# Performance work log

Measured on AMD Instinct MI355X. Metric: run time of the kernel, lower is better.

Reference implementation:

```python
import jax, jax.numpy as jnp
import numpy as np

EPS = 1e-12

def _l2norm(v):
    return v / (jnp.linalg.norm(v) + EPS)

def _spectral_norm_weight(W, u):
    # torch spectral_norm with n_power_iterations=1: v = norm(W^T u); u' = norm(W v);
    # sigma = u'^T W v with u', v detached; returns W / sigma.
    v = jax.lax.stop_gradient(_l2norm(W.T @ u))
    u2 = jax.lax.stop_gradient(_l2norm(W @ v))
    sigma = u2 @ (W @ v)
    return W / sigma

def setup_inputs() -> dict:
    key = jax.random.key(0)
    ks = jax.random.split(key, 8)
    C, H, W = 64, 96, 96
    Cfg = C // 8
    g = 1e-2  # small weight scale (module uses orthogonal init with tiny gain)
    return {
        "x":  jax.random.normal(ks[0], (1, C, H, W), jnp.float32),
        "Wf": jax.random.normal(ks[1], (Cfg, C), jnp.float32) * g,
        "bf": jnp.zeros((Cfg,), jnp.float32),
        "Wg": jax.random.normal(ks[2], (Cfg, C), jnp.float32) * g,
        "bg": jnp.zeros((Cfg,), jnp.float32),
        "Wh": jax.random.normal(ks[3], (C, C), jnp.float32) * g,
        "bh": jnp.zeros((C,), jnp.float32),
        "gamma": jax.random.normal(ks[4], (1,), jnp.float32),
        "uf": jax.random.normal(ks[5], (Cfg,), jnp.float32),
        "ug": jax.random.normal(ks[6], (Cfg,), jnp.float32),
        "uh": jax.random.normal(ks[7], (C,), jnp.float32),
    }

def reference(x, Wf, bf, Wg, bg, Wh, bh, gamma, uf, ug, uh):
    B, C, H, Wd = x.shape
    N = H * Wd
    xf = x.reshape(B, C, N)  # 1x1 convs act per-pixel -> matmul over channel dim
    Wf_sn = _spectral_norm_weight(Wf, uf)
    Wg_sn = _spectral_norm_weight(Wg, ug)
    Wh_sn = _spectral_norm_weight(Wh, uh)
    f_flat = jnp.einsum('oc,bcn->bon', Wf_sn, xf) + bf[:, None]  # [B,Cfg,N]
    g_flat = jnp.einsum('oc,bcn->bon', Wg_sn, xf) + bg[:, None]  # [B,Cfg,N]
    h_flat = jnp.einsum('oc,bcn->bon', Wh_sn, xf) + bh[:, None]  # [B,C,N]
    # s[b,n,m] = sum_k g[b,k,n] * f[b,k,m]  (g^T f)
    s = jnp.einsum('bkn,bkm->bnm', g_flat, f_flat)  # [B,N,N]
    beta = jax.nn.softmax(s, axis=1)                # softmax over dim=1 (g axis)
    o = jnp.einsum('bcn,bnm->bcm', h_flat, beta)    # [B,C,N]
    o = o.reshape(B, C, H, Wd)
    return gamma * o + x
```

## Files before the change

### kernel.cpp

```cpp
#include <hip/hip_runtime.h>
#include <hip/hip_bf16.h>

#define NPIX 9216
#define MTILES (NPIX / 16)

typedef __attribute__((ext_vector_type(4))) float f32x4;
typedef __attribute__((ext_vector_type(8))) short bf16x8;
typedef __attribute__((ext_vector_type(2))) unsigned int u32x2;

__device__ __forceinline__ void gload_lds16(const void* g, void* l) {
  __builtin_amdgcn_global_load_lds(
      (const __attribute__((address_space(1))) unsigned int*)g,
      (__attribute__((address_space(3))) unsigned int*)l, 16, 0, 0);
}
__device__ __forceinline__ void gload_lds4(const void* g, void* l) {
  __builtin_amdgcn_global_load_lds(
      (const __attribute__((address_space(1))) unsigned int*)g,
      (__attribute__((address_space(3))) unsigned int*)l, 4, 0, 0);
}
#define LDS_OFF(p) ((unsigned)(unsigned long long)(const __attribute__((address_space(3))) char*)(const char*)(p))

__global__ __launch_bounds__(256) void spectral_kernel(
    const float* __restrict__ Wf, const float* __restrict__ bfv,
    const float* __restrict__ Wg, const float* __restrict__ bgv,
    const float* __restrict__ Wh, const float* __restrict__ bhv,
    const float* __restrict__ uf, const float* __restrict__ ug,
    const float* __restrict__ uh,
    float* __restrict__ Wsc, float* __restrict__ bsc) {
  __shared__ float vsh3[3][64];
  __shared__ float is_s[3];
  const int tid = threadIdx.x;
  const int wv = tid >> 6, t = tid & 63;
  if (wv < 3) {
    const float* W = (wv == 0) ? Wf : (wv == 1) ? Wg : Wh;
    const float* u = (wv == 0) ? uf : (wv == 1) ? ug : uh;
    const int O = (wv == 2) ? 64 : 8;
    float v = 0.f;
    for (int o = 0; o < O; ++o) v += W[o * 64 + t] * u[o];
    float s = v * v;
    for (int off = 32; off; off >>= 1) s += __shfl_xor(s, off);
    vsh3[wv][t] = v / (sqrtf(s) + 1e-12f);
    float wvv = 0.f;
    if (t < O) { for (int c = 0; c < 64; ++c) wvv += W[t * 64 + c] * vsh3[wv][c]; }
    float s2 = (t < O) ? wvv * wvv : 0.f;
    for (int off = 32; off; off >>= 1) s2 += __shfl_xor(s2, off);
    const float nw = sqrtf(s2);
    if (t == 0) is_s[wv] = (nw + 1e-12f) / s2;
  }
  __syncthreads();
  const float sf = is_s[0] * 0.25f, sg = is_s[1], sh = is_s[2];
  for (int e = tid; e < 5120; e += 256) {
    const int r = e >> 6, c = e & 63;
    float val;
    if (r < 8)       val = Wf[r * 64 + c] * sf;
    else if (r < 16) val = Wg[(r - 8) * 64 + c] * sg;
    else             val = Wh[(r - 16) * 64 + c] * sh;
    Wsc[e] = val;
  }
  if (tid < 80) {
    bsc[tid] = (tid < 8) ? bfv[tid] * 0.25f
             : (tid < 16) ? bgv[tid - 8] : bhv[tid - 16];
  }
}

__global__ __launch_bounds__(256) void fgh_kernel(
    const float* __restrict__ x,
    const float* __restrict__ Wsc, const float* __restrict__ bsc,
    ushort* __restrict__ Qp, ushort* __restrict__ Kp, ushort* __restrict__ Vt2) {
  const int tid = threadIdx.x;
  const int px = tid & 63;
  const int rw = __builtin_amdgcn_readfirstlane(tid >> 6);
  const int r0 = blockIdx.y * 16 + rw * 4;
  const int p  = blockIdx.x * 64 + px;

  float xv[64];
  #pragma unroll
  for (int c = 0; c < 64; ++c) xv[c] = x[c * NPIX + p];

  float acc0 = 0.f, acc1 = 0.f, acc2 = 0.f, acc3 = 0.f;
  const float* w0 = Wsc + (r0 + 0) * 64;
  const float* w1 = Wsc + (r0 + 1) * 64;
  const float* w2 = Wsc + (r0 + 2) * 64;
  const float* w3 = Wsc + (r0 + 3) * 64;
  #pragma unroll
  for (int c = 0; c < 64; ++c) {
    const float xc = xv[c];
    acc0 += w0[c] * xc; acc1 += w1[c] * xc;
    acc2 += w2[c] * xc; acc3 += w3[c] * xc;
  }

  const int tile = p >> 5, nt = p & 31;
  const int tt = nt >> 4, gg = (nt >> 2) & 3, ii = nt & 3;
  const int kbase = tile * 512 + nt * 8;
  float accs[4] = {acc0, acc1, acc2, acc3};
  #pragma unroll
  for (int j = 0; j < 4; ++j) {
    const int r = r0 + j;
    const float val = accs[j] + bsc[r];
    if (r < 8) {
      const __hip_bfloat16 h = __float2bfloat16(val);
      const float hf = __bfloat162float(h);
      const __hip_bfloat16 lo = __float2bfloat16(val - hf);
      Qp[p * 16 + r]     = *(const ushort*)&h;
      Qp[p * 16 + 8 + r] = *(const ushort*)&lo;
    } else if (r < 16) {
      const int rk = r - 8;
      const __hip_bfloat16 h = __float2bfloat16(val);
      const float hf = __bfloat162float(h);
      const __hip_bfloat16 lo = __float2bfloat16(val - hf);
      Kp[kbase + rk]       = *(const ushort*)&h;
      Kp[kbase + 256 + rk] = *(const ushort*)&lo;
    } else {
      const int rv = r - 16;
      const __hip_bfloat16 hv = __float2bfloat16(val);
      const int idx = tile * 2048 +
          ((rv * 32 + gg * 8 + tt * 4 + ii) ^ (((rv >> 1) & 7) << 3));
      Vt2[idx] = *(const ushort*)&hv;
    }
  }
}

template <int S>
__global__ __launch_bounds__(256) void attn_kernel(
    const ushort* __restrict__ Qp, const ushort* __restrict__ Kp,
    const ushort* __restrict__ Vt2,
    ushort* __restrict__ Om,
    float* __restrict__ Sm) {
  constexpr int NSEG = NPIX / S;
  constexpr int NT = NSEG / 32;
  __shared__ ushort Vs[4][2048];
  __shared__ ushort Ks[4][512];
  const int tid  = threadIdx.x;
  const int w    = tid >> 6;
  const int l    = tid & 63;
  const int mloc = l & 15;
  const int g    = l >> 4;
  const int spl  = blockIdx.y;
  const int mrow = blockIdx.x * 64 + w * 16 + mloc;

  bf16x8 qh = *(const bf16x8*)(Qp + mrow * 16);
  bf16x8 ql = *(const bf16x8*)(Qp + mrow * 16 + 8);
  asm volatile("" : "+v"(qh), "+v"(ql));

  const int n0 = spl * NSEG;
  const char* vsrc = (const char*)Vt2 + ((size_t)(n0 >> 5)) * 4096 + w * 1024 + l * 16;
  const char* ksrc = (const char*)Kp + ((size_t)(n0 >> 5)) * 1024 + w * 256 + l * 4;

  #define STAGE(t_) do {                                                  \
    const int b_ = (t_) & 3;                                              \
    gload_lds16(vsrc + (size_t)(t_) * 4096, (char*)&Vs[b_][0] + w * 1024);\
    gload_lds4 (ksrc + (size_t)(t_) * 1024, (char*)&Ks[b_][0] + w * 256); \
  } while (0)

  STAGE(0);
  STAGE(1);

  const unsigned ks_base = LDS_OFF(&Ks[0][0]);
  const unsigned vs_base = LDS_OFF(&Vs[0][0]);
  const unsigned vswz = (mloc * 64 + g * 16) ^ (((mloc >> 1) & 7) << 4);

  float mx = -INFINITY, ls = 0.f;
  const f32x4 zero = {0.f, 0.f, 0.f, 0.f};
  f32x4 acc0 = zero, acc1 = zero, acc2 = zero, acc3 = zero;

  for (int t = 0; t < NT; ++t) {
    const int b = t & 3;
    if (t + 2 < NT) {
      STAGE(t + 2);
      asm volatile("s_waitcnt vmcnt(4)" ::: "memory");
    } else if (t + 1 < NT) {
      asm volatile("s_waitcnt vmcnt(2)" ::: "memory");
    } else {
      asm volatile("s_waitcnt vmcnt(0)" ::: "memory");
    }
    __builtin_amdgcn_s_barrier();

    const unsigned kaddr = ks_base + b * 1024 + mloc * 16;
    const unsigned vaddr = vs_base + b * 4096 + vswz;
    bf16x8 kh0, kl0, kh1, kl1, v0, v1, v2, v3;
    asm volatile("ds_read_b128 %0, %1"            : "=v"(kh0) : "v"(kaddr));
    asm volatile("ds_read_b128 %0, %1 offset:256" : "=v"(kh1) : "v"(kaddr));
    asm volatile("ds_read_b128 %0, %1 offset:512" : "=v"(kl0) : "v"(kaddr));
    asm volatile("ds_read_b128 %0, %1 offset:768" : "=v"(kl1) : "v"(kaddr));
    asm volatile("ds_read_b128 %0, %1"            : "=v"(v0)  : "v"(vaddr));
    asm volatile("ds_read_b128 %0, %1 offset:1024": "=v"(v1)  : "v"(vaddr));
    asm volatile("ds_read_b128 %0, %1 offset:2048": "=v"(v2)  : "v"(vaddr));
    asm volatile("ds_read_b128 %0, %1 offset:3072": "=v"(v3)  : "v"(vaddr));
    asm volatile("s_waitcnt lgkmcnt(0)" ::: "memory");
    __builtin_amdgcn_sched_barrier(0);

    f32x4 s0 = zero, s1 = zero;
    s0 = __builtin_amdgcn_mfma_f32_16x16x32_bf16(kh0, qh, s0, 0, 0, 0);
    s1 = __builtin_amdgcn_mfma_f32_16x16x32_bf16(kh1, qh, s1, 0, 0, 0);
    s0 = __builtin_amdgcn_mfma_f32_16x16x32_bf16(kh0, ql, s0, 0, 0, 0);
    s1 = __builtin_amdgcn_mfma_f32_16x16x32_bf16(kh1, ql, s1, 0, 0, 0);
    s0 = __builtin_amdgcn_mfma_f32_16x16x32_bf16(kl0, qh, s0, 0, 0, 0);
    s1 = __builtin_amdgcn_mfma_f32_16x16x32_bf16(kl1, qh, s1, 0, 0, 0);

    const float tm = fmaxf(
        fmaxf(fmaxf(s0[0], s0[1]), fmaxf(s0[2], s0[3])),
        fmaxf(fmaxf(s1[0], s1[1]), fmaxf(s1[2], s1[3])));
    if (__any(tm > mx + 8.0f)) {
      float tr = fmaxf(tm, __shfl_xor(tm, 16));
      tr = fmaxf(tr, __shfl_xor(tr, 32));
      const float mxn = fmaxf(mx, tr);
      const float corr = __expf(mx - mxn);
      ls *= corr;
      const float c0 = __shfl(corr, (g << 2) + 0);
      const float c1 = __shfl(corr, (g << 2) + 1);
      const float c2 = __shfl(corr, (g << 2) + 2);
      const float c3 = __shfl(corr, (g << 2) + 3);
      acc0[0] *= c0; acc0[1] *= c1; acc0[2] *= c2; acc0[3] *= c3;
      acc1[0] *= c0; acc1[1] *= c1; acc1[2] *= c2; acc1[3] *= c3;
      acc2[0] *= c0; acc2[1] *= c1; acc2[2] *= c2; acc2[3] *= c3;
      acc3[0] *= c0; acc3[1] *= c1; acc3[2] *= c2; acc3[3] *= c3;
      mx = mxn;
    }
    float pj[8];
    pj[0] = __expf(s0[0] - mx); pj[1] = __expf(s0[1] - mx);
    pj[2] = __expf(s0[2] - mx); pj[3] = __expf(s0[3] - mx);
    pj[4] = __expf(s1[0] - mx); pj[5] = __expf(s1[1] - mx);
    pj[6] = __expf(s1[2] - mx); pj[7] = __expf(s1[3] - mx);
    ls += ((pj[0] + pj[1]) + (pj[2] + pj[3])) + ((pj[4] + pj[5]) + (pj[6] + pj[7]));

    union { unsigned int u[4]; bf16x8 v; } pu;
    #pragma unroll
    for (int jj = 0; jj < 4; ++jj) {
      unsigned int r;
      asm("v_cvt_pk_bf16_f32 %0, %1, %2" : "=v"(r) : "v"(pj[2 * jj]), "v"(pj[2 * jj + 1]));
      pu.u[jj] = r;
    }
    acc0 = __builtin_amdgcn_mfma_f32_16x16x32_bf16(pu.v, v0, acc0, 0, 0, 0);
    acc1 = __builtin_amdgcn_mfma_f32_16x16x32_bf16(pu.v, v1, acc1, 0, 0, 0);
    acc2 = __builtin_amdgcn_mfma_f32_16x16x32_bf16(pu.v, v2, acc2, 0, 0, 0);
    acc3 = __builtin_amdgcn_mfma_f32_16x16x32_bf16(pu.v, v3, acc3, 0, 0, 0);
  }
  #undef STAGE

  ls += __shfl_xor(ls, 16);
  ls += __shfl_xor(ls, 32);

  const size_t mt = (size_t)blockIdx.x * 4 + w;
  ushort* Ob = Om + (mt * S + spl) * 1024;
  float*  Sb = Sm + (mt * S + spl) * 32;
  #pragma unroll
  for (int ct = 0; ct < 4; ++ct) {
    const f32x4 a = (ct == 0) ? acc0 : (ct == 1) ? acc1 : (ct == 2) ? acc2 : acc3;
    unsigned int r0, r1;
    asm("v_cvt_pk_bf16_f32 %0, %1, %2" : "=v"(r0) : "v"(a[0]), "v"(a[1]));
    asm("v_cvt_pk_bf16_f32 %0, %1, %2" : "=v"(r1) : "v"(a[2]), "v"(a[3]));
    u32x2 pk; pk[0] = r0; pk[1] = r1;
    *(u32x2*)(Ob + (ct * 16 + mloc) * 16 + 4 * g) = pk;
  }
  if (l < 16) { Sb[l] = mx; Sb[16 + l] = ls; }
}

template <int S>
__global__ __launch_bounds__(256) void combine_kernel(
    const ushort* __restrict__ Om, const float* __restrict__ Sm,
    const float* __restrict__ x, const float* __restrict__ gammap,
    float* __restrict__ out) {
  const int mt = blockIdx.x;
  const int m0 = mt * 16;
  const float gamma = gammap[0];
  const float* Sb = Sm + (size_t)mt * S * 32;
  const ushort* Ob = Om + (size_t)mt * S * 1024;
  for (int e = threadIdx.x; e < 1024; e += 256) {
    const int m = e & 15, c = e >> 4;
    float M = -INFINITY;
    #pragma unroll
    for (int s = 0; s < S; ++s) M = fmaxf(M, Sb[s * 32 + m]);
    float L = 0.f, val = 0.f;
    #pragma unroll
    for (int s = 0; s < S; ++s) {
      const float wgt = __expf(Sb[s * 32 + m] - M);
      L += Sb[s * 32 + 16 + m] * wgt;
      union { unsigned int i; float f; } cv;
      cv.i = ((unsigned int)Ob[s * 1024 + e]) << 16;
      val += cv.f * wgt;
    }
    const int idx = c * NPIX + m0 + m;
    out[idx] = gamma * (val / L) + x[idx];
  }
}

extern "C" void kernel_launch(void* const* d_in, const int* in_sizes, int n_in,
                              void* d_out, int out_size, void* d_ws, size_t ws_size,
                              hipStream_t stream) {
  const float* x     = (const float*)d_in[0];
  const float* Wf    = (const float*)d_in[1];
  const float* bf    = (const float*)d_in[2];
  const float* Wg    = (const float*)d_in[3];
  const float* bg    = (const float*)d_in[4];
  const float* Wh    = (const float*)d_in[5];
  const float* bh    = (const float*)d_in[6];
  const float* gamma = (const float*)d_in[7];
  const float* uf    = (const float*)d_in[8];
  const float* ug    = (const float*)d_in[9];
  const float* uh    = (const float*)d_in[10];
  float* out = (float*)d_out;

  char* ws = (char*)d_ws;
  float*  Wsc = (float*)(ws);
  float*  bsc = (float*)(ws + 20480);
  ushort* Qp  = (ushort*)(ws + 21504);
  ushort* Kp  = (ushort*)(ws + 21504 + NPIX * 16 * 2);
  ushort* Vt2 = (ushort*)(ws + 21504 + 2 * NPIX * 16 * 2);
  const size_t off = 21504 + (size_t)2 * NPIX * 16 * 2 + (size_t)NPIX * 64 * 2;
  ushort* Om = (ushort*)(ws + off);
  const size_t need16 = off + (size_t)MTILES * 16 * 1024 * 2 + (size_t)MTILES * 16 * 32 * 4;

  spectral_kernel<<<1, 256, 0, stream>>>(Wf, bf, Wg, bg, Wh, bh, uf, ug, uh, Wsc, bsc);
  fgh_kernel<<<dim3(NPIX / 64, 5), 256, 0, stream>>>(x, Wsc, bsc, Qp, Kp, Vt2);
  if (ws_size >= need16) {
    float* Sm = (float*)(ws + off + (size_t)MTILES * 16 * 1024 * 2);
    attn_kernel<16><<<dim3(NPIX / 64, 16), 256, 0, stream>>>(Qp, Kp, Vt2, Om, Sm);
    combine_kernel<16><<<MTILES, 256, 0, stream>>>(Om, Sm, x, gamma, out);
  } else {
    float* Sm = (float*)(ws + off + (size_t)MTILES * 8 * 1024 * 2);
    attn_kernel<8><<<dim3(NPIX / 64, 8), 256, 0, stream>>>(Qp, Kp, Vt2, Om, Sm);
    combine_kernel<8><<<MTILES, 256, 0, stream>>>(Om, Sm, x, gamma, out);
  }
}
```

Before: 77.60 us.

## Fuse spectral norm into projection, use exp2 softmax, split LDS wait, widen combine grid

Every projection block now recomputes the spectral-norm power iteration itself, which removes the separate single-block launch and the scaled-weight workspace round trip. Q is prescaled by log2(e) so the softmax and the combine step use exp2f, and the rescale threshold is adjusted to match. The attention loop now waits only for the K reads before the score MFMAs and waits for the V reads after the softmax, so LDS latency can overlap with the exp work. The combine kernel launches four times as many blocks, one element per thread. The cost is redundant spectral-norm work in every projection block.

```diff
diff --git a/kernel.cpp b/kernel.cpp
--- a/kernel.cpp
+++ b/kernel.cpp
@@ -20,13 +20,14 @@
 }
 #define LDS_OFF(p) ((unsigned)(unsigned long long)(const __attribute__((address_space(3))) char*)(const char*)(p))
 
-__global__ __launch_bounds__(256) void spectral_kernel(
+__global__ __launch_bounds__(256) void fgh_kernel(
+    const float* __restrict__ x,
     const float* __restrict__ Wf, const float* __restrict__ bfv,
     const float* __restrict__ Wg, const float* __restrict__ bgv,
     const float* __restrict__ Wh, const float* __restrict__ bhv,
     const float* __restrict__ uf, const float* __restrict__ ug,
     const float* __restrict__ uh,
-    float* __restrict__ Wsc, float* __restrict__ bsc) {
+    ushort* __restrict__ Qp, ushort* __restrict__ Kp, ushort* __restrict__ Vt2) {
   __shared__ float vsh3[3][64];
   __shared__ float is_s[3];
   const int tid = threadIdx.x;
@@ -48,26 +49,8 @@
     if (t == 0) is_s[wv] = (nw + 1e-12f) / s2;
   }
   __syncthreads();
-  const float sf = is_s[0] * 0.25f, sg = is_s[1], sh = is_s[2];
-  for (int e = tid; e < 5120; e += 256) {
-    const int r = e >> 6, c = e & 63;
-    float val;
-    if (r < 8)       val = Wf[r * 64 + c] * sf;
-    else if (r < 16) val = Wg[(r - 8) * 64 + c] * sg;
-    else             val = Wh[(r - 16) * 64 + c] * sh;
-    Wsc[e] = val;
-  }
-  if (tid < 80) {
-    bsc[tid] = (tid < 8) ? bfv[tid] * 0.25f
-             : (tid < 16) ? bgv[tid - 8] : bhv[tid - 16];
-  }
-}
-
-__global__ __launch_bounds__(256) void fgh_kernel(
-    const float* __restrict__ x,
-    const float* __restrict__ Wsc, const float* __restrict__ bsc,
-    ushort* __restrict__ Qp, ushort* __restrict__ Kp, ushort* __restrict__ Vt2) {
-  const int tid = threadIdx.x;
+
+  const float LOG2E = 1.44269504f;
   const int px = tid & 63;
   const int rw = __builtin_amdgcn_readfirstlane(tid >> 6);
   const int r0 = blockIdx.y * 16 + rw * 4;
@@ -77,27 +60,30 @@
   #pragma unroll
   for (int c = 0; c < 64; ++c) xv[c] = x[c * NPIX + p];
 
-  float acc0 = 0.f, acc1 = 0.f, acc2 = 0.f, acc3 = 0.f;
-  const float* w0 = Wsc + (r0 + 0) * 64;
-  const float* w1 = Wsc + (r0 + 1) * 64;
-  const float* w2 = Wsc + (r0 + 2) * 64;
-  const float* w3 = Wsc + (r0 + 3) * 64;
+  const float* W0;
+  float scl;
+  if (r0 < 8)       { W0 = Wf + r0 * 64;        scl = is_s[0]; }
+  else if (r0 < 16) { W0 = Wg + (r0 - 8) * 64;  scl = is_s[1]; }
+  else              { W0 = Wh + (r0 - 16) * 64; scl = is_s[2]; }
+
+  float acc[4] = {0.f, 0.f, 0.f, 0.f};
   #pragma unroll
   for (int c = 0; c < 64; ++c) {
     const float xc = xv[c];
-    acc0 += w0[c] * xc; acc1 += w1[c] * xc;
-    acc2 += w2[c] * xc; acc3 += w3[c] * xc;
+    acc[0] += W0[c]       * xc;
+    acc[1] += W0[64 + c]  * xc;
+    acc[2] += W0[128 + c] * xc;
+    acc[3] += W0[192 + c] * xc;
   }
 
   const int tile = p >> 5, nt = p & 31;
   const int tt = nt >> 4, gg = (nt >> 2) & 3, ii = nt & 3;
   const int kbase = tile * 512 + nt * 8;
-  float accs[4] = {acc0, acc1, acc2, acc3};
   #pragma unroll
   for (int j = 0; j < 4; ++j) {
     const int r = r0 + j;
-    const float val = accs[j] + bsc[r];
     if (r < 8) {
+      const float val = (acc[j] * scl + bfv[r]) * 0.25f * LOG2E;
       const __hip_bfloat16 h = __float2bfloat16(val);
       const float hf = __bfloat162float(h);
       const __hip_bfloat16 lo = __float2bfloat16(val - hf);
@@ -105,6 +91,7 @@
       Qp[p * 16 + 8 + r] = *(const ushort*)&lo;
     } else if (r < 16) {
       const int rk = r - 8;
+      const float val = acc[j] * scl + bgv[rk];
       const __hip_bfloat16 h = __float2bfloat16(val);
       const float hf = __bfloat162float(h);
       const __hip_bfloat16 lo = __float2bfloat16(val - hf);
@@ -112,12 +99,52 @@
       Kp[kbase + 256 + rk] = *(const ushort*)&lo;
     } else {
       const int rv = r - 16;
+      const float val = acc[j] * scl + bhv[rv];
       const __hip_bfloat16 hv = __float2bfloat16(val);
       const int idx = tile * 2048 +
           ((rv * 32 + gg * 8 + tt * 4 + ii) ^ (((rv >> 1) & 7) << 3));
       Vt2[idx] = *(const ushort*)&hv;
     }
   }
+}
+
+__device__ __forceinline__ void softmax_step(
+    const f32x4 s0, const f32x4 s1, int g, float& mx, float& ls,
+    f32x4& a0, f32x4& a1, f32x4& a2, f32x4& a3, bf16x8& pv) {
+  const float m1 = fmaxf(fmaxf(s0[0], s0[1]), s0[2]);
+  const float m2 = fmaxf(fmaxf(s0[3], s1[0]), s1[1]);
+  const float m3 = fmaxf(fmaxf(s1[2], s1[3]), m1);
+  const float tm = fmaxf(m2, m3);
+  if (__any(tm > mx + 11.5416f)) {
+    float tr = fmaxf(tm, __shfl_xor(tm, 16));
+    tr = fmaxf(tr, __shfl_xor(tr, 32));
+    const float mxn = fmaxf(mx, tr);
+    const float corr = exp2f(mx - mxn);
+    ls *= corr;
+    const float c0 = __shfl(corr, (g << 2) + 0);
+    const float c1 = __shfl(corr, (g << 2) + 1);
+    const float c2 = __shfl(corr, (g << 2) + 2);
+    const float c3 = __shfl(corr, (g << 2) + 3);
+    a0[0] *= c0; a0[1] *= c1; a0[2] *= c2; a0[3] *= c3;
+    a1[0] *= c0; a1[1] *= c1; a1[2] *= c2; a1[3] *= c3;
+    a2[0] *= c0; a2[1] *= c1; a2[2] *= c2; a2[3] *= c3;
+    a3[0] *= c0; a3[1] *= c1; a3[2] *= c2; a3[3] *= c3;
+    mx = mxn;
+  }
+  float pj[8];
+  pj[0] = exp2f(s0[0] - mx); pj[1] = exp2f(s0[1] - mx);
+  pj[2] = exp2f(s0[2] - mx); pj[3] = exp2f(s0[3] - mx);
+  pj[4] = exp2f(s1[0] - mx); pj[5] = exp2f(s1[1] - mx);
+  pj[6] = exp2f(s1[2] - mx); pj[7] = exp2f(s1[3] - mx);
+  ls += ((pj[0] + pj[1]) + (pj[2] + pj[3])) + ((pj[4] + pj[5]) + (pj[6] + pj[7]));
+  union { unsigned int u[4]; bf16x8 v; } pu;
+  #pragma unroll
+  for (int jj = 0; jj < 4; ++jj) {
+    unsigned int r;
+    asm("v_cvt_pk_bf16_f32 %0, %1, %2" : "=v"(r) : "v"(pj[2 * jj]), "v"(pj[2 * jj + 1]));
+    pu.u[jj] = r;
+  }
+  pv = pu.v;
 }
 
 template <int S>
@@ -186,7 +213,7 @@
     asm volatile("ds_read_b128 %0, %1 offset:1024": "=v"(v1)  : "v"(vaddr));
     asm volatile("ds_read_b128 %0, %1 offset:2048": "=v"(v2)  : "v"(vaddr));
     asm volatile("ds_read_b128 %0, %1 offset:3072": "=v"(v3)  : "v"(vaddr));
-    asm volatile("s_waitcnt lgkmcnt(0)" ::: "memory");
+    asm volatile("s_waitcnt lgkmcnt(4)" ::: "memory");
     __builtin_amdgcn_sched_barrier(0);
 
     f32x4 s0 = zero, s1 = zero;
@@ -197,43 +224,15 @@
     s0 = __builtin_amdgcn_mfma_f32_16x16x32_bf16(kl0, qh, s0, 0, 0, 0);
     s1 = __builtin_amdgcn_mfma_f32_16x16x32_bf16(kl1, qh, s1, 0, 0, 0);
 
-    const float tm = fmaxf(
-        fmaxf(fmaxf(s0[0], s0[1]), fmaxf(s0[2], s0[3])),
-        fmaxf(fmaxf(s1[0], s1[1]), fmaxf(s1[2], s1[3])));
-    if (__any(tm > mx + 8.0f)) {
-      float tr = fmaxf(tm, __shfl_xor(tm, 16));
-      tr = fmaxf(tr, __shfl_xor(tr, 32));
-      const float mxn = fmaxf(mx, tr);
-      const float corr = __expf(mx - mxn);
-      ls *= corr;
-      const float c0 = __shfl(corr, (g << 2) + 0);
-      const float c1 = __shfl(corr, (g << 2) + 1);
-      const float c2 = __shfl(corr, (g << 2) + 2);
-      const float c3 = __shfl(corr, (g << 2) + 3);
-      acc0[0] *= c0; acc0[1] *= c1; acc0[2] *= c2; acc0[3] *= c3;
-      acc1[0] *= c0; acc1[1] *= c1; acc1[2] *= c2; acc1[3] *= c3;
-      acc2[0] *= c0; acc2[1] *= c1; acc2[2] *= c2; acc2[3] *= c3;
-      acc3[0] *= c0; acc3[1] *= c1; acc3[2] *= c2; acc3[3] *= c3;
-      mx = mxn;
-    }
-    float pj[8];
-    pj[0] = __expf(s0[0] - mx); pj[1] = __expf(s0[1] - mx);
-    pj[2] = __expf(s0[2] - mx); pj[3] = __expf(s0[3] - mx);
-    pj[4] = __expf(s1[0] - mx); pj[5] = __expf(s1[1] - mx);
-    pj[6] = __expf(s1[2] - mx); pj[7] = __expf(s1[3] - mx);
-    ls += ((pj[0] + pj[1]) + (pj[2] + pj[3])) + ((pj[4] + pj[5]) + (pj[6] + pj[7]));
-
-    union { unsigned int u[4]; bf16x8 v; } pu;
-    #pragma unroll
-    for (int jj = 0; jj < 4; ++jj) {
-      unsigned int r;
-      asm("v_cvt_pk_bf16_f32 %0, %1, %2" : "=v"(r) : "v"(pj[2 * jj]), "v"(pj[2 * jj + 1]));
-      pu.u[jj] = r;
-    }
-    acc0 = __builtin_amdgcn_mfma_f32_16x16x32_bf16(pu.v, v0, acc0, 0, 0, 0);
-    acc1 = __builtin_amdgcn_mfma_f32_16x16x32_bf16(pu.v, v1, acc1, 0, 0, 0);
-    acc2 = __builtin_amdgcn_mfma_f32_16x16x32_bf16(pu.v, v2, acc2, 0, 0, 0);
-    acc3 = __builtin_amdgcn_mfma_f32_16x16x32_bf16(pu.v, v3, acc3, 0, 0, 0);
+    bf16x8 pv;
+    softmax_step(s0, s1, g, mx, ls, acc0, acc1, acc2, acc3, pv);
+
+    asm volatile("s_waitcnt lgkmcnt(0)" ::: "memory");
+    __builtin_amdgcn_sched_barrier(0);
+    acc0 = __builtin_amdgcn_mfma_f32_16x16x32_bf16(pv, v0, acc0, 0, 0, 0);
+    acc1 = __builtin_amdgcn_mfma_f32_16x16x32_bf16(pv, v1, acc1, 0, 0, 0);
+    acc2 = __builtin_amdgcn_mfma_f32_16x16x32_bf16(pv, v2, acc2, 0, 0, 0);
+    acc3 = __builtin_amdgcn_mfma_f32_16x16x32_bf16(pv, v3, acc3, 0, 0, 0);
   }
   #undef STAGE
 
@@ -260,28 +259,27 @@
     const ushort* __restrict__ Om, const float* __restrict__ Sm,
     const float* __restrict__ x, const float* __restrict__ gammap,
     float* __restrict__ out) {
-  const int mt = blockIdx.x;
+  const int mt = blockIdx.x >> 2;
   const int m0 = mt * 16;
+  const int e  = (blockIdx.x & 3) * 256 + threadIdx.x;
   const float gamma = gammap[0];
   const float* Sb = Sm + (size_t)mt * S * 32;
   const ushort* Ob = Om + (size_t)mt * S * 1024;
-  for (int e = threadIdx.x; e < 1024; e += 256) {
-    const int m = e & 15, c = e >> 4;
-    float M = -INFINITY;
-    #pragma unroll
-    for (int s = 0; s < S; ++s) M = fmaxf(M, Sb[s * 32 + m]);
-    float L = 0.f, val = 0.f;
-    #pragma unroll
-    for (int s = 0; s < S; ++s) {
-      const float wgt = __expf(Sb[s * 32 + m] - M);
-      L += Sb[s * 32 + 16 + m] * wgt;
-      union { unsigned int i; float f; } cv;
-      cv.i = ((unsigned int)Ob[s * 1024 + e]) << 16;
-      val += cv.f * wgt;
-    }
-    const int idx = c * NPIX + m0 + m;
-    out[idx] = gamma * (val / L) + x[idx];
-  }
+  const int m = e & 15, c = e >> 4;
+  float M = -INFINITY;
+  #pragma unroll
+  for (int s = 0; s < S; ++s) M = fmaxf(M, Sb[s * 32 + m]);
+  float L = 0.f, val = 0.f;
+  #pragma unroll
+  for (int s = 0; s < S; ++s) {
+    const float wgt = exp2f(Sb[s * 32 + m] - M);
+    L += Sb[s * 32 + 16 + m] * wgt;
+    union { unsigned int i; float f; } cv;
+    cv.i = ((unsigned int)Ob[s * 1024 + e]) << 16;
+    val += cv.f * wgt;
+  }
+  const int idx = c * NPIX + m0 + m;
+  out[idx] = gamma * (val / L) + x[idx];
 }
 
 extern "C" void kernel_launch(void* const* d_in, const int* in_sizes, int n_in,
@@ -301,24 +299,22 @@
   float* out = (float*)d_out;
 
   char* ws = (char*)d_ws;
-  float*  Wsc = (float*)(ws);
-  float*  bsc = (float*)(ws + 20480);
-  ushort* Qp  = (ushort*)(ws + 21504);
-  ushort* Kp  = (ushort*)(ws + 21504 + NPIX * 16 * 2);
-  ushort* Vt2 = (ushort*)(ws + 21504 + 2 * NPIX * 16 * 2);
-  const size_t off = 21504 + (size_t)2 * NPIX * 16 * 2 + (size_t)NPIX * 64 * 2;
+  ushort* Qp  = (ushort*)(ws + 256);
+  ushort* Kp  = (ushort*)(ws + 256 + NPIX * 16 * 2);
+  ushort* Vt2 = (ushort*)(ws + 256 + 2 * NPIX * 16 * 2);
+  const size_t off = 256 + (size_t)2 * NPIX * 16 * 2 + (size_t)NPIX * 64 * 2;
   ushort* Om = (ushort*)(ws + off);
   const size_t need16 = off + (size_t)MTILES * 16 * 1024 * 2 + (size_t)MTILES * 16 * 32 * 4;
 
-  spectral_kernel<<<1, 256, 0, stream>>>(Wf, bf, Wg, bg, Wh, bh, uf, ug, uh, Wsc, bsc);
-  fgh_kernel<<<dim3(NPIX / 64, 5), 256, 0, stream>>>(x, Wsc, bsc, Qp, Kp, Vt2);
+  fgh_kernel<<<dim3(NPIX / 64, 5), 256, 0, stream>>>(x, Wf, bf, Wg, bg, Wh, bh,
+                                                     uf, ug, uh, Qp, Kp, Vt2);
   if (ws_size >= need16) {
     float* Sm = (float*)(ws + off + (size_t)MTILES * 16 * 1024 * 2);
     attn_kernel<16><<<dim3(NPIX / 64, 16), 256, 0, stream>>>(Qp, Kp, Vt2, Om, Sm);
-    combine_kernel<16><<<MTILES, 256, 0, stream>>>(Om, Sm, x, gamma, out);
+    combine_kernel<16><<<MTILES * 4, 256, 0, stream>>>(Om, Sm, x, gamma, out);
   } else {
     float* Sm = (float*)(ws + off + (size_t)MTILES * 8 * 1024 * 2);
     attn_kernel<8><<<dim3(NPIX / 64, 8), 256, 0, stream>>>(Qp, Kp, Vt2, Om, Sm);
-    combine_kernel<8><<<MTILES, 256, 0, stream>>>(Om, Sm, x, gamma, out);
-  }
-}
+    combine_kernel<8><<<MTILES * 4, 256, 0, stream>>>(Om, Sm, x, gamma, out);
+  }
+}
```

Result: no change. 77.29 us (-0.4%).
